# Performance work log

Hardware: AMD Instinct MI355X
Metric: run time of the kernel (lower is better)

## Reference

```python
import jax, jax.numpy as jnp
import numpy as np
import math

N = 8192
IN_FEATURES = 512
OUT_FEATURES = 64
NEG_INF = -9e15

def setup_inputs() -> dict:
    key = jax.random.key(0)
    k1, k2, k3, k4 = jax.random.split(key, 4)
    inp = jax.random.normal(k1, (N, IN_FEATURES), dtype=jnp.float32)
    adj = jax.random.randint(k2, (N, N), 0, 2, dtype=jnp.int32)
    # xavier_uniform with gain=1.414 for [in, out] weights
    limit = 1.414 * math.sqrt(6.0 / (IN_FEATURES + OUT_FEATURES))
    kW = jax.random.uniform(k3, (IN_FEATURES, OUT_FEATURES), dtype=jnp.float32, minval=-limit, maxval=limit)
    vW = jax.random.uniform(k4, (IN_FEATURES, OUT_FEATURES), dtype=jnp.float32, minval=-limit, maxval=limit)
    return {"input": inp, "adj": adj, "kW": kW, "vW": vW}

def reference(input, adj, kW, vW):
    kh = input @ kW                      # [N, d]
    vh = input @ vW                      # [N, d]
    d = kh.shape[1]
    K = (kh @ kh.T) / jnp.sqrt(jnp.asarray(d, dtype=kh.dtype))  # [N, N]
    scores = jnp.where(adj > 0, K, jnp.asarray(NEG_INF, dtype=K.dtype))
    attention = jax.nn.softmax(scores, axis=1)
    # dropout is a no-op (p=0.0 / eval mode)
    h_prime = attention @ vh             # [N, d]
    return jax.nn.elu(h_prime)           # concat=True path
```

## Files before the change

kernel.cpp:

```cpp
#include <hip/hip_runtime.h>
#include <math.h>

typedef __bf16 bf16_t;
typedef __bf16 bf16x8 __attribute__((ext_vector_type(8)));
typedef float f32x4 __attribute__((ext_vector_type(4)));

#define NN 8192
#define L2E 1.44269504088896340736f
#define SMAX 45.0f
#define KSCALE 0.35355339059327373f
#define ACCW 66

__global__ __launch_bounds__(256) void proj_kernel(
    const float* __restrict__ input,
    const float* __restrict__ kW,
    const float* __restrict__ vW,
    bf16_t* __restrict__ khs_hi,
    bf16_t* __restrict__ khs_lo,
    bf16_t* __restrict__ vhT)
{
    __shared__ __align__(16) bf16_t WkH[64][136];
    __shared__ __align__(16) bf16_t WkL[64][136];
    __shared__ __align__(16) bf16_t WvH[64][136];
    __shared__ __align__(16) bf16_t WvL[64][136];

    const int tid   = threadIdx.x;
    const int wv    = tid >> 6;
    const int lane  = tid & 63;
    const int l15   = lane & 15;
    const int quad  = lane >> 4;
    const int rbase = blockIdx.x * 64 + wv * 16;

    f32x4 kacc[4] = {};
    f32x4 vacc[4] = {};

    for (int kk = 0; kk < 4; ++kk) {
        __syncthreads();
        #pragma unroll
        for (int i = 0; i < 32; ++i) {
            int idx = tid + i * 256;
            int kl  = idx >> 6;
            int n   = idx & 63;
            float wk  = kW[(kk * 128 + kl) * 64 + n];
            float wv2 = vW[(kk * 128 + kl) * 64 + n];
            bf16_t kh = (bf16_t)wk;
            bf16_t vh = (bf16_t)wv2;
            WkH[n][kl] = kh;  WkL[n][kl] = (bf16_t)(wk - (float)kh);
            WvH[n][kl] = vh;  WvL[n][kl] = (bf16_t)(wv2 - (float)vh);
        }
        __syncthreads();

        #pragma unroll
        for (int kc = 0; kc < 4; ++kc) {
            const float* ap = &input[(size_t)(rbase + l15) * 512 + kk * 128 + kc * 32 + quad * 8];
            f32x4 a0 = *(const f32x4*)ap;
            f32x4 a1 = *(const f32x4*)(ap + 4);
            bf16x8 ah, al;
            #pragma unroll
            for (int j = 0; j < 4; ++j) {
                bf16_t h0 = (bf16_t)a0[j], h1 = (bf16_t)a1[j];
                ah[j]     = h0;  al[j]     = (bf16_t)(a0[j] - (float)h0);
                ah[4 + j] = h1;  al[4 + j] = (bf16_t)(a1[j] - (float)h1);
            }
            #pragma unroll
            for (int nb = 0; nb < 4; ++nb) {
                bf16x8 bkh = *(const bf16x8*)&WkH[nb * 16 + l15][kc * 32 + quad * 8];
                bf16x8 bkl = *(const bf16x8*)&WkL[nb * 16 + l15][kc * 32 + quad * 8];
                bf16x8 bvh = *(const bf16x8*)&WvH[nb * 16 + l15][kc * 32 + quad * 8];
                bf16x8 bvl = *(const bf16x8*)&WvL[nb * 16 + l15][kc * 32 + quad * 8];
                kacc[nb] = __builtin_amdgcn_mfma_f32_16x16x32_bf16(ah, bkh, kacc[nb], 0, 0, 0);
                kacc[nb] = __builtin_amdgcn_mfma_f32_16x16x32_bf16(al, bkh, kacc[nb], 0, 0, 0);
                kacc[nb] = __builtin_amdgcn_mfma_f32_16x16x32_bf16(ah, bkl, kacc[nb], 0, 0, 0);
                vacc[nb] = __builtin_amdgcn_mfma_f32_16x16x32_bf16(ah, bvh, vacc[nb], 0, 0, 0);
                vacc[nb] = __builtin_amdgcn_mfma_f32_16x16x32_bf16(al, bvh, vacc[nb], 0, 0, 0);
                vacc[nb] = __builtin_amdgcn_mfma_f32_16x16x32_bf16(ah, bvl, vacc[nb], 0, 0, 0);
            }
        }
    }

    #pragma unroll
    for (int nb = 0; nb < 4; ++nb) {
        const int dcol = nb * 16 + l15;
        #pragma unroll
        for (int r = 0; r < 4; ++r) {
            float v  = kacc[nb][r] * KSCALE;
            bf16_t h = (bf16_t)v;
            khs_hi[(size_t)(rbase + quad * 4 + r) * 64 + dcol] = h;
            khs_lo[(size_t)(rbase + quad * 4 + r) * 64 + dcol] = (bf16_t)(v - (float)h);
        }
        union { bf16_t b[4]; uint2 u; } pk;
        #pragma unroll
        for (int r = 0; r < 4; ++r) pk.b[r] = (bf16_t)vacc[nb][r];
        *(uint2*)&vhT[(size_t)dcol * NN + rbase + quad * 4] = pk.u;
    }
}

__global__ __launch_bounds__(256) void bitpack(
    const int* __restrict__ adj, unsigned long long* __restrict__ mask64)
{
    const int gw   = (blockIdx.x * 256 + threadIdx.x) >> 6;
    const int lane = threadIdx.x & 63;
    const int* rp  = adj + (size_t)gw * NN + lane;
    unsigned long long* mp = mask64 + (size_t)gw * 128;
    #pragma unroll 8
    for (int g = 0; g < 128; ++g) {
        int v = rp[(size_t)g * 64];
        unsigned long long b = __ballot(v > 0);
        if (lane == 0) mp[g] = b;
    }
}

__global__ __launch_bounds__(256) void repack(
    const bf16_t* __restrict__ khs_hi, const bf16_t* __restrict__ vhT,
    bf16_t* __restrict__ ktile, bf16_t* __restrict__ vtile)
{
    int idx = blockIdx.x * 256 + threadIdx.x;
    int c    = idx & 65535;
    int t    = c >> 8;
    int rem  = c & 255;
    int f    = rem >> 6;
    int lane = rem & 63;
    int quad = lane >> 4;
    int l15  = lane & 15;
    if (idx < 65536) {
        int kperm = ((l15 >> 2) << 3) | (l15 & 3);
        int key = 32 * t + kperm + (f >> 1) * 4;
        int dim = (f & 1) * 32 + quad * 8;
        uint4 v = *(const uint4*)(khs_hi + (size_t)key * 64 + dim);
        *(uint4*)(ktile + (size_t)t * 2048 + f * 512 + lane * 8) = v;
    } else {
        uint4 v = *(const uint4*)(vhT + (size_t)(16 * f + l15) * NN + 32 * t + quad * 8);
        *(uint4*)(vtile + (size_t)t * 2048 + f * 512 + lane * 8) = v;
    }
}

__global__ void zero_acc(float* __restrict__ acc) {
    int i = blockIdx.x * blockDim.x + threadIdx.x;
    if (i < NN * ACCW) acc[i] = 0.f;
}

__global__ __launch_bounds__(512, 4) void attn_kernel(
    const unsigned int* __restrict__ mask,
    const bf16_t* __restrict__ khs_hi,
    const bf16_t* __restrict__ khs_lo,
    const bf16_t* __restrict__ ktile,
    const bf16_t* __restrict__ vtile,
    float* __restrict__ acc)
{
    __shared__ __align__(16) float Msl[4 * 16 * 68];

    const int tid   = threadIdx.x;
    const int w     = tid >> 6;
    const int lane  = tid & 63;
    const int l15   = lane & 15;
    const int quad  = lane >> 4;
    const int rb    = blockIdx.x >> 1;
    const int ch    = blockIdx.x & 1;
    const int qbase = rb * 16;
    const int tile0 = ch * 128 + w * 16;

    const bf16x8 qh0 = *(const bf16x8*)&khs_hi[(size_t)(qbase + l15) * 64 + quad * 8];
    const bf16x8 qh1 = *(const bf16x8*)&khs_hi[(size_t)(qbase + l15) * 64 + 32 + quad * 8];
    const bf16x8 ql0 = *(const bf16x8*)&khs_lo[(size_t)(qbase + l15) * 64 + quad * 8];
    const bf16x8 ql1 = *(const bf16x8*)&khs_lo[(size_t)(qbase + l15) * 64 + 32 + quad * 8];

    bf16x8 ones;
    #pragma unroll
    for (int j = 0; j < 8; ++j) ones[j] = (bf16_t)1.0f;

    const uint4* mrow = (const uint4*)(mask + (size_t)(qbase + l15) * 256 + tile0);

    f32x4 o0 = {}, o1 = {}, o2 = {}, o3 = {}, o4 = {};

    const bf16_t* kbase = ktile + (size_t)tile0 * 2048 + lane * 8;
    const bf16_t* vbase = vtile + (size_t)tile0 * 2048 + lane * 8;

    for (int t0 = 0; t0 < 4; ++t0) {
        uint4 mw4 = mrow[t0];
        #pragma unroll
        for (int u = 0; u < 4; ++u) {
            const int t = t0 * 4 + u;
            const unsigned int word = (&mw4.x)[u];
            const bf16_t* kp = kbase + (size_t)t * 2048;
            const bf16_t* vp = vbase + (size_t)t * 2048;

            bf16x8 a00 = *(const bf16x8*)(kp);
            bf16x8 a01 = *(const bf16x8*)(kp + 512);
            bf16x8 a10 = *(const bf16x8*)(kp + 1024);
            bf16x8 a11 = *(const bf16x8*)(kp + 1536);
            bf16x8 bv0 = *(const bf16x8*)(vp);
            bf16x8 bv1 = *(const bf16x8*)(vp + 512);
            bf16x8 bv2 = *(const bf16x8*)(vp + 1024);
            bf16x8 bv3 = *(const bf16x8*)(vp + 1536);

            f32x4 zz = {};
            f32x4 c0 = __builtin_amdgcn_mfma_f32_16x16x32_bf16(a00, qh0, zz, 0, 0, 0);
            c0 = __builtin_amdgcn_mfma_f32_16x16x32_bf16(a01, qh1, c0, 0, 0, 0);
            c0 = __builtin_amdgcn_mfma_f32_16x16x32_bf16(a00, ql0, c0, 0, 0, 0);
            c0 = __builtin_amdgcn_mfma_f32_16x16x32_bf16(a01, ql1, c0, 0, 0, 0);
            f32x4 c1 = __builtin_amdgcn_mfma_f32_16x16x32_bf16(a10, qh0, zz, 0, 0, 0);
            c1 = __builtin_amdgcn_mfma_f32_16x16x32_bf16(a11, qh1, c1, 0, 0, 0);
            c1 = __builtin_amdgcn_mfma_f32_16x16x32_bf16(a10, ql0, c1, 0, 0, 0);
            c1 = __builtin_amdgcn_mfma_f32_16x16x32_bf16(a11, ql1, c1, 0, 0, 0);

            bf16x8 pa;
            #pragma unroll
            for (int r = 0; r < 4; ++r) {
                float p0 = ((word >> (8 * quad + r)) & 1u)
                             ? __builtin_amdgcn_exp2f((c0[r] - SMAX) * L2E) : 0.f;
                float p1 = ((word >> (8 * quad + 4 + r)) & 1u)
                             ? __builtin_amdgcn_exp2f((c1[r] - SMAX) * L2E) : 0.f;
                pa[r]     = (bf16_t)p0;
                pa[4 + r] = (bf16_t)p1;
            }

            o0 = __builtin_amdgcn_mfma_f32_16x16x32_bf16(pa, bv0, o0, 0, 0, 0);
            o1 = __builtin_amdgcn_mfma_f32_16x16x32_bf16(pa, bv1, o1, 0, 0, 0);
            o2 = __builtin_amdgcn_mfma_f32_16x16x32_bf16(pa, bv2, o2, 0, 0, 0);
            o3 = __builtin_amdgcn_mfma_f32_16x16x32_bf16(pa, bv3, o3, 0, 0, 0);
            o4 = __builtin_amdgcn_mfma_f32_16x16x32_bf16(pa, ones, o4, 0, 0, 0);
        }
    }

    float* M = Msl;
    #pragma unroll
    for (int s = 4; s >= 1; s >>= 1) {
        __syncthreads();
        if (w >= s && w < 2 * s) {
            float* base = M + (w - s) * 16 * 68;
            #pragma unroll
            for (int r = 0; r < 4; ++r) {
                const int row = quad * 4 + r;
                base[row * 68 + l15]      = o0[r];
                base[row * 68 + 16 + l15] = o1[r];
                base[row * 68 + 32 + l15] = o2[r];
                base[row * 68 + 48 + l15] = o3[r];
                if (l15 == 0) base[row * 68 + 64] = o4[r];
            }
        }
        __syncthreads();
        if (w < s) {
            float* base = M + w * 16 * 68;
            #pragma unroll
            for (int r = 0; r < 4; ++r) {
                const int row = quad * 4 + r;
                o0[r] += base[row * 68 + l15];
                o1[r] += base[row * 68 + 16 + l15];
                o2[r] += base[row * 68 + 32 + l15];
                o3[r] += base[row * 68 + 48 + l15];
                o4[r] += base[row * 68 + 64];
            }
        }
    }

    if (w == 0) {
        #pragma unroll
        for (int r = 0; r < 4; ++r) {
            const size_t row = (size_t)qbase + quad * 4 + r;
            atomicAdd(&acc[row * ACCW + l15],      o0[r]);
            atomicAdd(&acc[row * ACCW + 16 + l15], o1[r]);
            atomicAdd(&acc[row * ACCW + 32 + l15], o2[r]);
            atomicAdd(&acc[row * ACCW + 48 + l15], o3[r]);
            if (l15 == 0) atomicAdd(&acc[row * ACCW + 64], o4[r]);
        }
    }
}

__global__ void finalize(const float* __restrict__ acc, float* __restrict__ out) {
    int i = blockIdx.x * blockDim.x + threadIdx.x;
    int row = i >> 6, d = i & 63;
    float l = acc[(size_t)row * ACCW + 64];
    float v = acc[(size_t)row * ACCW + d] / (l > 0.f ? l : 1.f);
    out[i] = v > 0.f ? v : expm1f(v);
}

extern "C" void kernel_launch(void* const* d_in, const int* in_sizes, int n_in,
                              void* d_out, int out_size, void* d_ws, size_t ws_size,
                              hipStream_t stream) {
    const float* input = nullptr;
    const int*   adj   = nullptr;
    const float* kW    = nullptr;
    const float* vW    = nullptr;
    for (int i = 0; i < n_in; ++i) {
        if (in_sizes[i] == 8192 * 512)            input = (const float*)d_in[i];
        else if (in_sizes[i] == 512 * 64) {
            if (!kW) kW = (const float*)d_in[i]; else vW = (const float*)d_in[i];
        } else                                    adj = (const int*)d_in[i];
    }
    float* out = (float*)d_out;

    char* ws = (char*)d_ws;
    bf16_t* khs_hi = (bf16_t*)ws;
    bf16_t* khs_lo = (bf16_t*)(ws + 1u * 1024 * 1024);
    bf16_t* vhT    = (bf16_t*)(ws + 2u * 1024 * 1024);
    float*  acc    = (float*)(ws + 3u * 1024 * 1024);
    unsigned long long* mask64 = (unsigned long long*)(ws + 6u * 1024 * 1024);
    bf16_t* ktile  = (bf16_t*)(ws + 14u * 1024 * 1024);
    bf16_t* vtile  = (bf16_t*)(ws + 15u * 1024 * 1024);

    zero_acc<<<(NN * ACCW + 255) / 256, 256, 0, stream>>>(acc);
    proj_kernel<<<128, 256, 0, stream>>>(input, kW, vW, khs_hi, khs_lo, vhT);
    bitpack<<<2048, 256, 0, stream>>>(adj, mask64);
    repack<<<512, 256, 0, stream>>>(khs_hi, vhT, ktile, vtile);
    attn_kernel<<<1024, 512, 0, stream>>>((const unsigned int*)mask64, khs_hi, khs_lo,
                                          ktile, vtile, acc);
    finalize<<<(NN * 64) / 512, 512, 0, stream>>>(acc, out);
}
```

Baseline: 528.3 us.

## Fuse adjacency bitpacking and finalize into attention kernel, drop atomics

```diff
diff --git a/kernel.cpp b/kernel.cpp
--- a/kernel.cpp
+++ b/kernel.cpp
@@ -9,7 +9,6 @@
 #define L2E 1.44269504088896340736f
 #define SMAX 45.0f
 #define KSCALE 0.35355339059327373f
-#define ACCW 66
 
 __global__ __launch_bounds__(256) void proj_kernel(
     const float* __restrict__ input,
@@ -92,21 +91,6 @@
         #pragma unroll
         for (int r = 0; r < 4; ++r) pk.b[r] = (bf16_t)vacc[nb][r];
         *(uint2*)&vhT[(size_t)dcol * NN + rbase + quad * 4] = pk.u;
-    }
-}
-
-__global__ __launch_bounds__(256) void bitpack(
-    const int* __restrict__ adj, unsigned long long* __restrict__ mask64)
-{
-    const int gw   = (blockIdx.x * 256 + threadIdx.x) >> 6;
-    const int lane = threadIdx.x & 63;
-    const int* rp  = adj + (size_t)gw * NN + lane;
-    unsigned long long* mp = mask64 + (size_t)gw * 128;
-    #pragma unroll 8
-    for (int g = 0; g < 128; ++g) {
-        int v = rp[(size_t)g * 64];
-        unsigned long long b = __ballot(v > 0);
-        if (lane == 0) mp[g] = b;
     }
 }
 
@@ -134,30 +118,38 @@
     }
 }
 
-__global__ void zero_acc(float* __restrict__ acc) {
-    int i = blockIdx.x * blockDim.x + threadIdx.x;
-    if (i < NN * ACCW) acc[i] = 0.f;
-}
-
 __global__ __launch_bounds__(512, 4) void attn_kernel(
-    const unsigned int* __restrict__ mask,
+    const int* __restrict__ adj,
     const bf16_t* __restrict__ khs_hi,
     const bf16_t* __restrict__ khs_lo,
     const bf16_t* __restrict__ ktile,
     const bf16_t* __restrict__ vtile,
-    float* __restrict__ acc)
+    float* __restrict__ out)
 {
-    __shared__ __align__(16) float Msl[4 * 16 * 68];
+    __shared__ __align__(16) unsigned int ShBuf[8 * 544];
 
     const int tid   = threadIdx.x;
     const int w     = tid >> 6;
     const int lane  = tid & 63;
     const int l15   = lane & 15;
     const int quad  = lane >> 4;
-    const int rb    = blockIdx.x >> 1;
-    const int ch    = blockIdx.x & 1;
-    const int qbase = rb * 16;
-    const int tile0 = ch * 128 + w * 16;
+    const int qbase = blockIdx.x * 16;
+
+    {
+        #pragma unroll 2
+        for (int r2 = 0; r2 < 2; ++r2) {
+            const int row = 2 * w + r2;
+            const int* rp = adj + (size_t)(qbase + row) * NN + lane;
+            #pragma unroll 8
+            for (int g = 0; g < 128; ++g) {
+                int v = rp[g * 64];
+                unsigned long long b = __ballot(v > 0);
+                if (lane == 0)
+                    *(unsigned long long*)&ShBuf[(g >> 4) * 544 + row * 34 + ((2 * g) & 31)] = b;
+            }
+        }
+    }
+    __syncthreads();
 
     const bf16x8 qh0 = *(const bf16x8*)&khs_hi[(size_t)(qbase + l15) * 64 + quad * 8];
     const bf16x8 qh1 = *(const bf16x8*)&khs_hi[(size_t)(qbase + l15) * 64 + 32 + quad * 8];
@@ -168,61 +160,56 @@
     #pragma unroll
     for (int j = 0; j < 8; ++j) ones[j] = (bf16_t)1.0f;
 
-    const uint4* mrow = (const uint4*)(mask + (size_t)(qbase + l15) * 256 + tile0);
-
     f32x4 o0 = {}, o1 = {}, o2 = {}, o3 = {}, o4 = {};
 
-    const bf16_t* kbase = ktile + (size_t)tile0 * 2048 + lane * 8;
-    const bf16_t* vbase = vtile + (size_t)tile0 * 2048 + lane * 8;
-
-    for (int t0 = 0; t0 < 4; ++t0) {
-        uint4 mw4 = mrow[t0];
-        #pragma unroll
-        for (int u = 0; u < 4; ++u) {
-            const int t = t0 * 4 + u;
-            const unsigned int word = (&mw4.x)[u];
-            const bf16_t* kp = kbase + (size_t)t * 2048;
-            const bf16_t* vp = vbase + (size_t)t * 2048;
-
-            bf16x8 a00 = *(const bf16x8*)(kp);
-            bf16x8 a01 = *(const bf16x8*)(kp + 512);
-            bf16x8 a10 = *(const bf16x8*)(kp + 1024);
-            bf16x8 a11 = *(const bf16x8*)(kp + 1536);
-            bf16x8 bv0 = *(const bf16x8*)(vp);
-            bf16x8 bv1 = *(const bf16x8*)(vp + 512);
-            bf16x8 bv2 = *(const bf16x8*)(vp + 1024);
-            bf16x8 bv3 = *(const bf16x8*)(vp + 1536);
-
-            f32x4 zz = {};
-            f32x4 c0 = __builtin_amdgcn_mfma_f32_16x16x32_bf16(a00, qh0, zz, 0, 0, 0);
-            c0 = __builtin_amdgcn_mfma_f32_16x16x32_bf16(a01, qh1, c0, 0, 0, 0);
-            c0 = __builtin_amdgcn_mfma_f32_16x16x32_bf16(a00, ql0, c0, 0, 0, 0);
-            c0 = __builtin_amdgcn_mfma_f32_16x16x32_bf16(a01, ql1, c0, 0, 0, 0);
-            f32x4 c1 = __builtin_amdgcn_mfma_f32_16x16x32_bf16(a10, qh0, zz, 0, 0, 0);
-            c1 = __builtin_amdgcn_mfma_f32_16x16x32_bf16(a11, qh1, c1, 0, 0, 0);
-            c1 = __builtin_amdgcn_mfma_f32_16x16x32_bf16(a10, ql0, c1, 0, 0, 0);
-            c1 = __builtin_amdgcn_mfma_f32_16x16x32_bf16(a11, ql1, c1, 0, 0, 0);
-
-            bf16x8 pa;
-            #pragma unroll
-            for (int r = 0; r < 4; ++r) {
-                float p0 = ((word >> (8 * quad + r)) & 1u)
-                             ? __builtin_amdgcn_exp2f((c0[r] - SMAX) * L2E) : 0.f;
-                float p1 = ((word >> (8 * quad + 4 + r)) & 1u)
-                             ? __builtin_amdgcn_exp2f((c1[r] - SMAX) * L2E) : 0.f;
-                pa[r]     = (bf16_t)p0;
-                pa[4 + r] = (bf16_t)p1;
-            }
-
-            o0 = __builtin_amdgcn_mfma_f32_16x16x32_bf16(pa, bv0, o0, 0, 0, 0);
-            o1 = __builtin_amdgcn_mfma_f32_16x16x32_bf16(pa, bv1, o1, 0, 0, 0);
-            o2 = __builtin_amdgcn_mfma_f32_16x16x32_bf16(pa, bv2, o2, 0, 0, 0);
-            o3 = __builtin_amdgcn_mfma_f32_16x16x32_bf16(pa, bv3, o3, 0, 0, 0);
-            o4 = __builtin_amdgcn_mfma_f32_16x16x32_bf16(pa, ones, o4, 0, 0, 0);
-        }
-    }
-
-    float* M = Msl;
+    const unsigned int* mrow = &ShBuf[w * 544 + l15 * 34];
+    const bf16_t* kbase = ktile + (size_t)(w * 32) * 2048 + lane * 8;
+    const bf16_t* vbase = vtile + (size_t)(w * 32) * 2048 + lane * 8;
+
+    #pragma unroll 4
+    for (int t = 0; t < 32; ++t) {
+        const unsigned int word = mrow[t];
+        const bf16_t* kp = kbase + (size_t)t * 2048;
+        const bf16_t* vp = vbase + (size_t)t * 2048;
+
+        bf16x8 a00 = *(const bf16x8*)(kp);
+        bf16x8 a01 = *(const bf16x8*)(kp + 512);
+        bf16x8 a10 = *(const bf16x8*)(kp + 1024);
+        bf16x8 a11 = *(const bf16x8*)(kp + 1536);
+        bf16x8 bv0 = *(const bf16x8*)(vp);
+        bf16x8 bv1 = *(const bf16x8*)(vp + 512);
+        bf16x8 bv2 = *(const bf16x8*)(vp + 1024);
+        bf16x8 bv3 = *(const bf16x8*)(vp + 1536);
+
+        f32x4 zz = {};
+        f32x4 c0 = __builtin_amdgcn_mfma_f32_16x16x32_bf16(a00, qh0, zz, 0, 0, 0);
+        c0 = __builtin_amdgcn_mfma_f32_16x16x32_bf16(a01, qh1, c0, 0, 0, 0);
+        c0 = __builtin_amdgcn_mfma_f32_16x16x32_bf16(a00, ql0, c0, 0, 0, 0);
+        c0 = __builtin_amdgcn_mfma_f32_16x16x32_bf16(a01, ql1, c0, 0, 0, 0);
+        f32x4 c1 = __builtin_amdgcn_mfma_f32_16x16x32_bf16(a10, qh0, zz, 0, 0, 0);
+        c1 = __builtin_amdgcn_mfma_f32_16x16x32_bf16(a11, qh1, c1, 0, 0, 0);
+        c1 = __builtin_amdgcn_mfma_f32_16x16x32_bf16(a10, ql0, c1, 0, 0, 0);
+        c1 = __builtin_amdgcn_mfma_f32_16x16x32_bf16(a11, ql1, c1, 0, 0, 0);
+
+        bf16x8 pa;
+        #pragma unroll
+        for (int r = 0; r < 4; ++r) {
+            float p0 = ((word >> (8 * quad + r)) & 1u)
+                         ? __builtin_amdgcn_exp2f((c0[r] - SMAX) * L2E) : 0.f;
+            float p1 = ((word >> (8 * quad + 4 + r)) & 1u)
+                         ? __builtin_amdgcn_exp2f((c1[r] - SMAX) * L2E) : 0.f;
+            pa[r]     = (bf16_t)p0;
+            pa[4 + r] = (bf16_t)p1;
+        }
+
+        o0 = __builtin_amdgcn_mfma_f32_16x16x32_bf16(pa, bv0, o0, 0, 0, 0);
+        o1 = __builtin_amdgcn_mfma_f32_16x16x32_bf16(pa, bv1, o1, 0, 0, 0);
+        o2 = __builtin_amdgcn_mfma_f32_16x16x32_bf16(pa, bv2, o2, 0, 0, 0);
+        o3 = __builtin_amdgcn_mfma_f32_16x16x32_bf16(pa, bv3, o3, 0, 0, 0);
+        o4 = __builtin_amdgcn_mfma_f32_16x16x32_bf16(pa, ones, o4, 0, 0, 0);
+    }
+
+    float* M = (float*)ShBuf;
     #pragma unroll
     for (int s = 4; s >= 1; s >>= 1) {
         __syncthreads();
@@ -256,22 +243,20 @@
     if (w == 0) {
         #pragma unroll
         for (int r = 0; r < 4; ++r) {
-            const size_t row = (size_t)qbase + quad * 4 + r;
-            atomicAdd(&acc[row * ACCW + l15],      o0[r]);
-            atomicAdd(&acc[row * ACCW + 16 + l15], o1[r]);
-            atomicAdd(&acc[row * ACCW + 32 + l15], o2[r]);
-            atomicAdd(&acc[row * ACCW + 48 + l15], o3[r]);
-            if (l15 == 0) atomicAdd(&acc[row * ACCW + 64], o4[r]);
-        }
-    }
-}
-
-__global__ void finalize(const float* __restrict__ acc, float* __restrict__ out) {
-    int i = blockIdx.x * blockDim.x + threadIdx.x;
-    int row = i >> 6, d = i & 63;
-    float l = acc[(size_t)row * ACCW + 64];
-    float v = acc[(size_t)row * ACCW + d] / (l > 0.f ? l : 1.f);
-    out[i] = v > 0.f ? v : expm1f(v);
+            const float l   = o4[r];
+            const float inv = l > 0.f ? 1.0f / l : 0.f;
+            float v0 = o0[r] * inv, v1 = o1[r] * inv, v2 = o2[r] * inv, v3 = o3[r] * inv;
+            v0 = v0 > 0.f ? v0 : expm1f(v0);
+            v1 = v1 > 0.f ? v1 : expm1f(v1);
+            v2 = v2 > 0.f ? v2 : expm1f(v2);
+            v3 = v3 > 0.f ? v3 : expm1f(v3);
+            float* op = &out[(size_t)(qbase + quad * 4 + r) * 64 + l15];
+            op[0]  = v0;
+            op[16] = v1;
+            op[32] = v2;
+            op[48] = v3;
+        }
+    }
 }
 
 extern "C" void kernel_launch(void* const* d_in, const int* in_sizes, int n_in,
@@ -293,16 +278,10 @@
     bf16_t* khs_hi = (bf16_t*)ws;
     bf16_t* khs_lo = (bf16_t*)(ws + 1u * 1024 * 1024);
     bf16_t* vhT    = (bf16_t*)(ws + 2u * 1024 * 1024);
-    float*  acc    = (float*)(ws + 3u * 1024 * 1024);
-    unsigned long long* mask64 = (unsigned long long*)(ws + 6u * 1024 * 1024);
-    bf16_t* ktile  = (bf16_t*)(ws + 14u * 1024 * 1024);
-    bf16_t* vtile  = (bf16_t*)(ws + 15u * 1024 * 1024);
-
-    zero_acc<<<(NN * ACCW + 255) / 256, 256, 0, stream>>>(acc);
+    bf16_t* ktile  = (bf16_t*)(ws + 3u * 1024 * 1024);
+    bf16_t* vtile  = (bf16_t*)(ws + 4u * 1024 * 1024);
+
     proj_kernel<<<128, 256, 0, stream>>>(input, kW, vW, khs_hi, khs_lo, vhT);
-    bitpack<<<2048, 256, 0, stream>>>(adj, mask64);
     repack<<<512, 256, 0, stream>>>(khs_hi, vhT, ktile, vtile);
-    attn_kernel<<<1024, 512, 0, stream>>>((const unsigned int*)mask64, khs_hi, khs_lo,
-                                          ktile, vtile, acc);
-    finalize<<<(NN * 64) / 512, 512, 0, stream>>>(acc, out);
-}
+    attn_kernel<<<512, 512, 0, stream>>>(adj, khs_hi, khs_lo, ktile, vtile, out);
+}
```

After: 556.8 us. +5.4%, slower.
